# Kernel tuning notes

Measured on AMD Instinct MI355X. Metric: run time of the kernel, lower is better.

The kernel has to match this reference:

```python
import jax, jax.numpy as jnp
import numpy as np

N = 50000
E = 800000
IN_CH = 128
HID = 64
HEADS = 4
NEG_SLOPE_GAT = 0.2   # PyG GATConv default negative_slope
NEG_SLOPE_ACT = 0.01  # nn.LeakyReLU default
LN_EPS = 1e-5


def segment_softmax(logits, seg, num):
    # softmax over edges grouped by destination node (PyG softmax semantics)
    m = jax.ops.segment_max(logits, seg, num_segments=num)
    m = jnp.where(jnp.isfinite(m), m, 0.0)
    e = jnp.exp(logits - m[seg])
    s = jax.ops.segment_sum(e, seg, num_segments=num)
    return e / (s[seg] + 1e-16)


def gat_conv(x, edge_index, W, a_src, a_dst, b, heads, out_ch):
    n = x.shape[0]
    loop = jnp.arange(n)
    src = jnp.concatenate([edge_index[0], loop])  # message sources (x_j)
    dst = jnp.concatenate([edge_index[1], loop])  # aggregation targets (x_i)
    h = (x @ W).reshape(n, heads, out_ch)          # [N,H,C]
    alpha_src = (h * a_src).sum(-1)                # [N,H]
    alpha_dst = (h * a_dst).sum(-1)                # [N,H]
    alpha = alpha_src[src] + alpha_dst[dst]        # [E',H]
    alpha = jax.nn.leaky_relu(alpha, NEG_SLOPE_GAT)
    alpha = segment_softmax(alpha, dst, n)
    msg = h[src] * alpha[:, :, None]               # [E',H,C] gathered messages
    out = jax.ops.segment_sum(msg, dst, num_segments=n)  # [N,H,C]
    return out.reshape(n, heads * out_ch) + b


def layer_norm(x, gamma, beta):
    mu = x.mean(-1, keepdims=True)
    var = ((x - mu) ** 2).mean(-1, keepdims=True)
    return (x - mu) * jax.lax.rsqrt(var + LN_EPS) * gamma + beta


def setup_inputs() -> dict:
    key = jax.random.key(0)
    ks = jax.random.split(key, 12)
    d1 = HEADS * HID
    inp = {
        "x": jax.random.normal(ks[0], (N, IN_CH), dtype=jnp.float32),
        "edge_index": jax.random.randint(ks[1], (2, E), 0, N, dtype=jnp.int64),
        "W1": jax.random.normal(ks[2], (IN_CH, d1), dtype=jnp.float32) * 0.05,
        "a_src1": jax.random.normal(ks[3], (HEADS, HID), dtype=jnp.float32) * 0.1,
        "a_dst1": jax.random.normal(ks[4], (HEADS, HID), dtype=jnp.float32) * 0.1,
        "b1": jnp.zeros((d1,), dtype=jnp.float32),
        "gamma": jnp.ones((d1,), dtype=jnp.float32),
        "beta": jnp.zeros((d1,), dtype=jnp.float32),
        "W2": jax.random.normal(ks[5], (d1, HID), dtype=jnp.float32) * 0.05,
        "a_src2": jax.random.normal(ks[6], (1, HID), dtype=jnp.float32) * 0.1,
        "a_dst2": jax.random.normal(ks[7], (1, HID), dtype=jnp.float32) * 0.1,
        "b2": jnp.zeros((HID,), dtype=jnp.float32),
    }
    return inp


def reference(x, edge_index, W1, a_src1, a_dst1, b1, gamma, beta, W2, a_src2, a_dst2, b2):
    h = gat_conv(x, edge_index, W1, a_src1, a_dst1, b1, HEADS, HID)  # [N, H*HID]
    h = layer_norm(h, gamma, beta)
    h = jax.nn.leaky_relu(h, NEG_SLOPE_ACT)
    out = gat_conv(h, edge_index, W2, a_src2, a_dst2, b2, 1, HID)    # [N, HID]
    return out
```

## Files before the change

### kernel.cpp

```cpp
#include <hip/hip_runtime.h>
#include <hip/hip_bf16.h>

#define IN_CH 128
#define D1 256
#define HID 64
#define HEADS 4
#define SCAN_BLK 1024

typedef _Float16 h16;
typedef __attribute__((ext_vector_type(4))) _Float16 half4v;
typedef __attribute__((ext_vector_type(8))) _Float16 half8v;
typedef __attribute__((ext_vector_type(4))) float f32x4;

__device__ __forceinline__ float lrelu02(float v) { return v > 0.f ? v : 0.2f * v; }
__device__ __forceinline__ float lrelu001(float v) { return v > 0.f ? v : 0.01f * v; }

__global__ __launch_bounds__(256) void setup_kernel(const float* __restrict__ W1,
                                                    const float* __restrict__ W2,
                                                    const float* __restrict__ a_src1,
                                                    const float* __restrict__ a_dst1,
                                                    const float* __restrict__ a_src2,
                                                    const float* __restrict__ a_dst2,
                                                    const int* __restrict__ ei,
                                                    int* __restrict__ cnt,
                                                    h16* __restrict__ w1t,
                                                    h16* __restrict__ w2t,
                                                    int nE) {
    const int b = blockIdx.x;
    const int t = threadIdx.x;
    if (b == 0) {
        for (int k = 0; k < IN_CH; ++k) w1t[t * IN_CH + k] = (h16)W1[k * D1 + t];
    } else if (b == 1) {
        if (t < HID)
            for (int k = 0; k < D1; ++k) w2t[t * D1 + k] = (h16)W2[k * HID + t];
        for (int i = t; i < 14 * D1; i += 256) w2t[66 * D1 + i] = (h16)0.f;
    } else if (b == 2) {
        for (int o = t; o < 1024; o += 256) {
            int v = o >> 7, k = o & 127;
            int h = v & 3;
            const float* avec = (v >> 2) ? (a_dst1 + h * HID) : (a_src1 + h * HID);
            const float* wrow = W1 + k * D1 + h * HID;
            float s = 0.f;
            for (int c = 0; c < HID; ++c) s += wrow[c] * avec[c];
            w1t[(256 + v) * IN_CH + k] = (h16)s;
            w1t[(264 + v) * IN_CH + k] = (h16)0.f;
        }
    } else if (b == 3) {
        for (int o = t; o < 512; o += 256) {
            int v = o >> 8, k = o & 255;
            const float* avec = v ? a_dst2 : a_src2;
            const float* wrow = W2 + k * HID;
            float s = 0.f;
            for (int c = 0; c < HID; ++c) s += wrow[c] * avec[c];
            w2t[(64 + v) * D1 + k] = (h16)s;
        }
    } else {
        int e = (b - 4) * 256 + t;
        if (e < nE) atomicAdd(&cnt[ei[nE + e]], 1);
    }
}

__global__ __launch_bounds__(256) void scan1_kernel(const int* __restrict__ cnt,
                                                    int* __restrict__ pre,
                                                    int* __restrict__ blockSums, int n) {
    __shared__ int lds[256];
    const int t = threadIdx.x;
    const int base = blockIdx.x * SCAN_BLK + t * 4;
    int v0 = 0, v1 = 0, v2 = 0, v3 = 0;
    if (base + 0 < n) v0 = cnt[base + 0];
    if (base + 1 < n) v1 = cnt[base + 1];
    if (base + 2 < n) v2 = cnt[base + 2];
    if (base + 3 < n) v3 = cnt[base + 3];
    int s = v0 + v1 + v2 + v3;
    lds[t] = s;
    __syncthreads();
    for (int off = 1; off < 256; off <<= 1) {
        int x = 0;
        if (t >= off) x = lds[t - off];
        __syncthreads();
        if (t >= off) lds[t] += x;
        __syncthreads();
    }
    int excl = lds[t] - s;
    if (t == 255) blockSums[blockIdx.x] = lds[255];
    if (base + 0 < n) pre[base + 0] = excl;
    if (base + 1 < n) pre[base + 1] = excl + v0;
    if (base + 2 < n) pre[base + 2] = excl + v0 + v1;
    if (base + 3 < n) pre[base + 3] = excl + v0 + v1 + v2;
}

__global__ __launch_bounds__(256) void scan23_kernel(int* __restrict__ pre,
                                                     const int* __restrict__ blockSums,
                                                     int* __restrict__ cursor,
                                                     int n, int nE, int nb) {
    __shared__ int soff_s;
    const int t = threadIdx.x;
    if (t < 64) {
        int v = (t < blockIdx.x && t < nb) ? blockSums[t] : 0;
        #pragma unroll
        for (int off = 1; off < 64; off <<= 1) v += __shfl_xor(v, off, 64);
        if (t == 0) soff_s = v;
    }
    __syncthreads();
    const int soff = soff_s;
    const int base = blockIdx.x * SCAN_BLK + t * 4;
    #pragma unroll
    for (int q = 0; q < 4; ++q) {
        int i = base + q;
        if (i < n) {
            int v = pre[i] + soff;
            pre[i] = v;
            cursor[i] = v;
        }
    }
    if (blockIdx.x == 0 && t == 0) pre[n] = nE;
}

__global__ __launch_bounds__(256) void scatter_ewt_kernel(const int* __restrict__ ei,
                                                          int* __restrict__ cursor,
                                                          const float* __restrict__ asad,
                                                          int* __restrict__ srcIdx,
                                                          h16* __restrict__ wE1, int nE) {
    int e = blockIdx.x * 256 + threadIdx.x;
    if (e >= nE) return;
    int src = ei[e];
    int dst = ei[nE + e];
    int pos = atomicAdd(&cursor[dst], 1);
    srcIdx[pos] = src;
    float4 as = *(const float4*)&asad[(size_t)src * 8];
    float4 ad = *(const float4*)&asad[(size_t)dst * 8 + 4];
    half4v w;
    w.x = (h16)expf(lrelu02(as.x + ad.x));
    w.y = (h16)expf(lrelu02(as.y + ad.y));
    w.z = (h16)expf(lrelu02(as.z + ad.z));
    w.w = (h16)expf(lrelu02(as.w + ad.w));
    *(half4v*)&wE1[(size_t)pos * 4] = w;
}

__global__ __launch_bounds__(256) void gemm1_mfma(const float* __restrict__ x,
                                                  const h16* __restrict__ w1t,
                                                  h16* __restrict__ h1,
                                                  float* __restrict__ asad, int n) {
    const int wave = threadIdx.x >> 6, lane = threadIdx.x & 63;
    const int r = lane & 15, ksel = lane >> 4;
    const int rowBase = blockIdx.x * 64 + wave * 16;
    const int row_a = rowBase + r;
    half8v a[4];
    if (row_a < n) {
        const float* xrow = x + (size_t)row_a * IN_CH + ksel * 8;
        #pragma unroll
        for (int kk = 0; kk < 4; ++kk) {
            float4 u = *(const float4*)(xrow + kk * 32);
            float4 v = *(const float4*)(xrow + kk * 32 + 4);
            half8v av;
            av[0] = (h16)u.x; av[1] = (h16)u.y; av[2] = (h16)u.z; av[3] = (h16)u.w;
            av[4] = (h16)v.x; av[5] = (h16)v.y; av[6] = (h16)v.z; av[7] = (h16)v.w;
            a[kk] = av;
        }
    } else {
        #pragma unroll
        for (int kk = 0; kk < 4; ++kk) a[kk] = (half8v){};
    }
    f32x4 acc[17];
    #pragma unroll
    for (int ct = 0; ct < 17; ++ct) acc[ct] = (f32x4){0.f, 0.f, 0.f, 0.f};
    #pragma unroll
    for (int ct = 0; ct < 17; ++ct) {
        const h16* wrow = w1t + (size_t)(ct * 16 + r) * IN_CH + ksel * 8;
        #pragma unroll
        for (int kk = 0; kk < 4; ++kk) {
            half8v b = *(const half8v*)(wrow + kk * 32);
            acc[ct] = __builtin_amdgcn_mfma_f32_16x16x32_f16(a[kk], b, acc[ct], 0, 0, 0);
        }
    }
    #pragma unroll
    for (int i = 0; i < 4; ++i) {
        int row = rowBase + ksel * 4 + i;
        if (row < n) {
            #pragma unroll
            for (int ct = 0; ct < 16; ++ct)
                h1[(size_t)row * D1 + ct * 16 + r] = (h16)acc[ct][i];
            if (r < 8) asad[(size_t)row * 8 + r] = acc[16][i];
        }
    }
}

__global__ __launch_bounds__(256) void gemm2_mfma(const h16* __restrict__ hm,
                                                  const h16* __restrict__ w2t,
                                                  h16* __restrict__ h2,
                                                  float* __restrict__ asad2, int n) {
    const int wave = threadIdx.x >> 6, lane = threadIdx.x & 63;
    const int r = lane & 15, ksel = lane >> 4;
    const int rowBase = blockIdx.x * 64 + wave * 16;
    const h16* xrow = hm + (size_t)(rowBase + r) * D1 + ksel * 8;
    half8v a[8];
    #pragma unroll
    for (int kk = 0; kk < 8; ++kk) a[kk] = *(const half8v*)(xrow + kk * 32);
    f32x4 acc[5];
    #pragma unroll
    for (int ct = 0; ct < 5; ++ct) acc[ct] = (f32x4){0.f, 0.f, 0.f, 0.f};
    #pragma unroll
    for (int ct = 0; ct < 5; ++ct) {
        const h16* wrow = w2t + (size_t)(ct * 16 + r) * D1 + ksel * 8;
        #pragma unroll
        for (int kk = 0; kk < 8; ++kk) {
            half8v b = *(const half8v*)(wrow + kk * 32);
            acc[ct] = __builtin_amdgcn_mfma_f32_16x16x32_f16(a[kk], b, acc[ct], 0, 0, 0);
        }
    }
    #pragma unroll
    for (int i = 0; i < 4; ++i) {
        int row = rowBase + ksel * 4 + i;
        if (row < n) {
            #pragma unroll
            for (int ct = 0; ct < 4; ++ct)
                h2[(size_t)row * HID + ct * 16 + r] = (h16)acc[ct][i];
            if (r < 2) asad2[(size_t)row * 2 + r] = acc[4][i];
        }
    }
}

__global__ __launch_bounds__(256) void gather1_kernel(const h16* __restrict__ h1,
                                                      const float* __restrict__ asad,
                                                      const h16* __restrict__ wE1,
                                                      const int* __restrict__ rowStart,
                                                      const int* __restrict__ srcIdx,
                                                      const float* __restrict__ b1,
                                                      const float* __restrict__ gamma,
                                                      const float* __restrict__ beta,
                                                      h16* __restrict__ hmid, int n, int npad) {
    const int lane = threadIdx.x & 63;
    const int node = (blockIdx.x * 256 + threadIdx.x) >> 6;
    if (node >= npad) return;
    if (node >= n) {
        half4v z = {};
        *(half4v*)&hmid[(size_t)node * D1 + lane * 4] = z;
        return;
    }
    const int hh = lane >> 4;
    const float w = expf(lrelu02(asad[(size_t)node * 8 + hh] +
                                 asad[(size_t)node * 8 + 4 + hh]));
    half4v sv = *(const half4v*)&h1[(size_t)node * D1 + lane * 4];
    float4 acc = make_float4((float)sv.x * w, (float)sv.y * w,
                             (float)sv.z * w, (float)sv.w * w);
    float den = w;
    const int beg = rowStart[node], end = rowStart[node + 1];
    int j = beg;
    for (; j + 7 < end; j += 8) {
        int sI[8]; float wv[8]; half4v rv[8];
        #pragma unroll
        for (int q = 0; q < 8; ++q) sI[q] = srcIdx[j + q];
        #pragma unroll
        for (int q = 0; q < 8; ++q) wv[q] = (float)wE1[(size_t)(j + q) * 4 + hh];
        #pragma unroll
        for (int q = 0; q < 8; ++q) rv[q] = *(const half4v*)&h1[(size_t)sI[q] * D1 + lane * 4];
        #pragma unroll
        for (int q = 0; q < 8; ++q) {
            acc.x = fmaf((float)rv[q].x, wv[q], acc.x);
            acc.y = fmaf((float)rv[q].y, wv[q], acc.y);
            acc.z = fmaf((float)rv[q].z, wv[q], acc.z);
            acc.w = fmaf((float)rv[q].w, wv[q], acc.w);
            den += wv[q];
        }
    }
    for (; j + 3 < end; j += 4) {
        int sI[4]; float wv[4]; half4v rv[4];
        #pragma unroll
        for (int q = 0; q < 4; ++q) sI[q] = srcIdx[j + q];
        #pragma unroll
        for (int q = 0; q < 4; ++q) wv[q] = (float)wE1[(size_t)(j + q) * 4 + hh];
        #pragma unroll
        for (int q = 0; q < 4; ++q) rv[q] = *(const half4v*)&h1[(size_t)sI[q] * D1 + lane * 4];
        #pragma unroll
        for (int q = 0; q < 4; ++q) {
            acc.x = fmaf((float)rv[q].x, wv[q], acc.x);
            acc.y = fmaf((float)rv[q].y, wv[q], acc.y);
            acc.z = fmaf((float)rv[q].z, wv[q], acc.z);
            acc.w = fmaf((float)rv[q].w, wv[q], acc.w);
            den += wv[q];
        }
    }
    for (; j < end; ++j) {
        int s = srcIdx[j];
        float wj = (float)wE1[(size_t)j * 4 + hh];
        half4v xv = *(const half4v*)&h1[(size_t)s * D1 + lane * 4];
        acc.x = fmaf((float)xv.x, wj, acc.x);
        acc.y = fmaf((float)xv.y, wj, acc.y);
        acc.z = fmaf((float)xv.z, wj, acc.z);
        acc.w = fmaf((float)xv.w, wj, acc.w);
        den += wj;
    }
    float inv = 1.f / (den + 1e-16f);
    float4 bv = *(const float4*)&b1[lane * 4];
    float4 y;
    y.x = acc.x * inv + bv.x; y.y = acc.y * inv + bv.y;
    y.z = acc.z * inv + bv.z; y.w = acc.w * inv + bv.w;
    float s = y.x + y.y + y.z + y.w;
    #pragma unroll
    for (int off = 1; off < 64; off <<= 1) s += __shfl_xor(s, off, 64);
    float mu = s * (1.f / 256.f);
    float4 dx;
    dx.x = y.x - mu; dx.y = y.y - mu; dx.z = y.z - mu; dx.w = y.w - mu;
    float sq = dx.x * dx.x + dx.y * dx.y + dx.z * dx.z + dx.w * dx.w;
    #pragma unroll
    for (int off = 1; off < 64; off <<= 1) sq += __shfl_xor(sq, off, 64);
    float rs = rsqrtf(sq * (1.f / 256.f) + 1e-5f);
    float4 g = *(const float4*)&gamma[lane * 4];
    float4 be = *(const float4*)&beta[lane * 4];
    half4v o;
    o.x = (h16)lrelu001(dx.x * rs * g.x + be.x);
    o.y = (h16)lrelu001(dx.y * rs * g.y + be.y);
    o.z = (h16)lrelu001(dx.z * rs * g.z + be.z);
    o.w = (h16)lrelu001(dx.w * rs * g.w + be.w);
    *(half4v*)&hmid[(size_t)node * D1 + lane * 4] = o;
}

__global__ __launch_bounds__(256) void gather2_kernel(const h16* __restrict__ h2,
                                                      const float* __restrict__ asad2,
                                                      const int* __restrict__ rowStart,
                                                      const int* __restrict__ srcIdx,
                                                      const float* __restrict__ b2,
                                                      float* __restrict__ out, int n) {
    const int lane = threadIdx.x & 63;
    const int node = (blockIdx.x * 256 + threadIdx.x) >> 6;
    if (node >= n) return;
    const int li = lane & 15, eh = lane >> 4;
    const int c0 = li * 4;
    const float ad_n = asad2[(size_t)node * 2 + 1];
    float acc[4] = {0.f, 0.f, 0.f, 0.f};
    float den = 0.f;
    if (eh == 0) {
        float w0 = expf(lrelu02(asad2[(size_t)node * 2] + ad_n));
        half4v sv = *(const half4v*)&h2[(size_t)node * HID + c0];
        #pragma unroll
        for (int i = 0; i < 4; ++i) acc[i] = (float)sv[i] * w0;
        den = w0;
    }
    const int beg = rowStart[node], end = rowStart[node + 1];
    int j = beg;
    for (; j + 7 < end; j += 8) {
        int e0 = j + eh, e1 = j + 4 + eh;
        int s0 = srcIdx[e0], s1 = srcIdx[e1];
        float a0 = asad2[(size_t)s0 * 2], a1 = asad2[(size_t)s1 * 2];
        half4v r0 = *(const half4v*)&h2[(size_t)s0 * HID + c0];
        half4v r1 = *(const half4v*)&h2[(size_t)s1 * HID + c0];
        float w0 = expf(lrelu02(a0 + ad_n));
        float w1 = expf(lrelu02(a1 + ad_n));
        #pragma unroll
        for (int i = 0; i < 4; ++i) {
            acc[i] = fmaf((float)r0[i], w0, acc[i]);
            acc[i] = fmaf((float)r1[i], w1, acc[i]);
        }
        den += w0 + w1;
    }
    for (; j < end; j += 4) {
        int e = j + eh;
        bool v = e < end;
        int s = v ? srcIdx[e] : 0;
        float w = v ? expf(lrelu02(asad2[(size_t)s * 2] + ad_n)) : 0.f;
        half4v r = *(const half4v*)&h2[(size_t)s * HID + c0];
        #pragma unroll
        for (int i = 0; i < 4; ++i) acc[i] = fmaf((float)r[i], w, acc[i]);
        den += w;
    }
    #pragma unroll
    for (int i = 0; i < 4; ++i) {
        acc[i] += __shfl_xor(acc[i], 32, 64);
        acc[i] += __shfl_xor(acc[i], 16, 64);
    }
    den += __shfl_xor(den, 32, 64);
    den += __shfl_xor(den, 16, 64);
    if (lane < 16) {
        float inv = 1.f / (den + 1e-16f);
        float4 bv = *(const float4*)&b2[c0];
        float4 o;
        o.x = acc[0] * inv + bv.x;
        o.y = acc[1] * inv + bv.y;
        o.z = acc[2] * inv + bv.z;
        o.w = acc[3] * inv + bv.w;
        *(float4*)&out[(size_t)node * HID + c0] = o;
    }
}

extern "C" void kernel_launch(void* const* d_in, const int* in_sizes, int n_in,
                              void* d_out, int out_size, void* d_ws, size_t ws_size,
                              hipStream_t stream) {
    const float* x      = (const float*)d_in[0];
    const int*   ei     = (const int*)d_in[1];
    const float* W1     = (const float*)d_in[2];
    const float* a_src1 = (const float*)d_in[3];
    const float* a_dst1 = (const float*)d_in[4];
    const float* b1     = (const float*)d_in[5];
    const float* gamma  = (const float*)d_in[6];
    const float* beta   = (const float*)d_in[7];
    const float* W2     = (const float*)d_in[8];
    const float* a_src2 = (const float*)d_in[9];
    const float* a_dst2 = (const float*)d_in[10];
    const float* b2     = (const float*)d_in[11];
    float* out = (float*)d_out;

    const int N = in_sizes[0] / IN_CH;
    const int E = in_sizes[1] / 2;
    const int NP = (N + 63) & ~63;

    float* ws = (float*)d_ws;
    size_t off = 0;
    h16*   h1   = (h16*)(ws + off); off += (size_t)128 * N;
    h16*   hmid = (h16*)(ws + off); off += (size_t)128 * NP;
    h16*   h2   = (h16*)(ws + off); off += (size_t)32 * N;
    float* asad = ws + off;         off += (size_t)8 * N;
    float* asad2= ws + off;         off += (size_t)2 * N;
    h16*   wE1  = (h16*)(ws + off); off += (size_t)2 * E;
    int* srcIdx    = (int*)(ws + off); off += E;
    int* rowStart  = (int*)(ws + off); off += N + 1;
    int* cursor    = (int*)(ws + off); off += N;
    int* blockSums = (int*)(ws + off); off += 64;
    h16* w1t = (h16*)(ws + off); off += 17408;
    h16* w2t = (h16*)(ws + off); off += 10240;

    const int nodeBlocks  = (N + 3) / 4;
    const int nodeBlocksP = (NP + 3) / 4;
    const int nThreadBlocksE = (E + 255) / 256;
    const int scanBlocks = (N + SCAN_BLK - 1) / SCAN_BLK;

    hipMemsetAsync(cursor, 0, (size_t)N * 4, stream);
    setup_kernel<<<4 + nThreadBlocksE, 256, 0, stream>>>(
        W1, W2, a_src1, a_dst1, a_src2, a_dst2, ei, cursor, w1t, w2t, E);
    scan1_kernel<<<scanBlocks, 256, 0, stream>>>(cursor, rowStart, blockSums, N);
    scan23_kernel<<<scanBlocks, 256, 0, stream>>>(rowStart, blockSums, cursor, N, E, scanBlocks);

    gemm1_mfma<<<NP / 64, 256, 0, stream>>>(x, w1t, h1, asad, N);
    scatter_ewt_kernel<<<nThreadBlocksE, 256, 0, stream>>>(ei, cursor, asad, srcIdx, wE1, E);
    gather1_kernel<<<nodeBlocksP, 256, 0, stream>>>(h1, asad, wE1, rowStart, srcIdx,
                                                    b1, gamma, beta, hmid, N, NP);
    gemm2_mfma<<<NP / 64, 256, 0, stream>>>(hmid, w2t, h2, asad2, N);
    gather2_kernel<<<nodeBlocks, 256, 0, stream>>>(h2, asad2, rowStart, srcIdx,
                                                   b2, out, N);
}
```

Measured before the change: 261.6 us.

## Pad CSR rows to multiples of four, fuse scan with gemm1, use fp16 gather accumulation

Each destination row in the CSR is padded to a multiple of four edges. Padding slots point to a dummy node n, whose zeroed features and -1e30 logit make its weight vanish, so the gather loops can use vector int4 index loads with no tail predication. The scan fixup kernel and the gemm1 kernel are merged into one launch. Edge weights move to a head-major layout so half4 weight loads are contiguous. Gather1 accumulates products and the denominator in packed fp16 to cut ALU work, which risks precision loss and overflow for high-degree nodes. The memset grows to clear the padded index and weight buffers.

```diff
diff --git a/kernel.cpp b/kernel.cpp
--- a/kernel.cpp
+++ b/kernel.cpp
@@ -67,10 +67,10 @@
     const int t = threadIdx.x;
     const int base = blockIdx.x * SCAN_BLK + t * 4;
     int v0 = 0, v1 = 0, v2 = 0, v3 = 0;
-    if (base + 0 < n) v0 = cnt[base + 0];
-    if (base + 1 < n) v1 = cnt[base + 1];
-    if (base + 2 < n) v2 = cnt[base + 2];
-    if (base + 3 < n) v3 = cnt[base + 3];
+    if (base + 0 < n) v0 = (cnt[base + 0] + 3) & ~3;
+    if (base + 1 < n) v1 = (cnt[base + 1] + 3) & ~3;
+    if (base + 2 < n) v2 = (cnt[base + 2] + 3) & ~3;
+    if (base + 3 < n) v3 = (cnt[base + 3] + 3) & ~3;
     int s = v0 + v1 + v2 + v3;
     lds[t] = s;
     __syncthreads();
@@ -89,38 +89,94 @@
     if (base + 3 < n) pre[base + 3] = excl + v0 + v1 + v2;
 }
 
-__global__ __launch_bounds__(256) void scan23_kernel(int* __restrict__ pre,
-                                                     const int* __restrict__ blockSums,
-                                                     int* __restrict__ cursor,
-                                                     int n, int nE, int nb) {
-    __shared__ int soff_s;
-    const int t = threadIdx.x;
-    if (t < 64) {
-        int v = (t < blockIdx.x && t < nb) ? blockSums[t] : 0;
-        #pragma unroll
-        for (int off = 1; off < 64; off <<= 1) v += __shfl_xor(v, off, 64);
-        if (t == 0) soff_s = v;
-    }
-    __syncthreads();
-    const int soff = soff_s;
-    const int base = blockIdx.x * SCAN_BLK + t * 4;
-    #pragma unroll
-    for (int q = 0; q < 4; ++q) {
-        int i = base + q;
-        if (i < n) {
-            int v = pre[i] + soff;
-            pre[i] = v;
-            cursor[i] = v;
-        }
-    }
-    if (blockIdx.x == 0 && t == 0) pre[n] = nE;
+__global__ __launch_bounds__(256) void scan23_gemm1_kernel(
+        int* __restrict__ pre, const int* __restrict__ blockSums,
+        int* __restrict__ cursor, int* __restrict__ srcIdx,
+        float* __restrict__ asad2, int n, int nbScan,
+        const float* __restrict__ x, const h16* __restrict__ w1t,
+        h16* __restrict__ h1, float* __restrict__ asad) {
+    if (blockIdx.x < (unsigned)nbScan) {
+        __shared__ int soff_s;
+        const int t = threadIdx.x;
+        if (t < 64) {
+            int v = (t < (int)blockIdx.x && t < nbScan) ? blockSums[t] : 0;
+            #pragma unroll
+            for (int off = 1; off < 64; off <<= 1) v += __shfl_xor(v, off, 64);
+            if (t == 0) soff_s = v;
+        }
+        __syncthreads();
+        const int soff = soff_s;
+        const int base = blockIdx.x * SCAN_BLK + t * 4;
+        #pragma unroll
+        for (int q = 0; q < 4; ++q) {
+            int i = base + q;
+            if (i < n) {
+                int d = cursor[i];
+                int v = pre[i] + soff;
+                pre[i] = v;
+                cursor[i] = v;
+                int dp = (d + 3) & ~3;
+                for (int p = d; p < dp; ++p) srcIdx[v + p] = n;
+                if (i == n - 1) pre[n] = v + dp;
+            }
+        }
+        if (blockIdx.x == 0 && t == 0) {
+            asad2[(size_t)n * 2] = -1e30f;
+            asad2[(size_t)n * 2 + 1] = -1e30f;
+        }
+        return;
+    }
+    const int bid = blockIdx.x - nbScan;
+    const int wave = threadIdx.x >> 6, lane = threadIdx.x & 63;
+    const int r = lane & 15, ksel = lane >> 4;
+    const int rowBase = bid * 64 + wave * 16;
+    const int row_a = rowBase + r;
+    half8v a[4];
+    if (row_a < n) {
+        const float* xrow = x + (size_t)row_a * IN_CH + ksel * 8;
+        #pragma unroll
+        for (int kk = 0; kk < 4; ++kk) {
+            float4 u = *(const float4*)(xrow + kk * 32);
+            float4 v = *(const float4*)(xrow + kk * 32 + 4);
+            half8v av;
+            av[0] = (h16)u.x; av[1] = (h16)u.y; av[2] = (h16)u.z; av[3] = (h16)u.w;
+            av[4] = (h16)v.x; av[5] = (h16)v.y; av[6] = (h16)v.z; av[7] = (h16)v.w;
+            a[kk] = av;
+        }
+    } else {
+        #pragma unroll
+        for (int kk = 0; kk < 4; ++kk) a[kk] = (half8v){};
+    }
+    f32x4 acc[17];
+    #pragma unroll
+    for (int ct = 0; ct < 17; ++ct) acc[ct] = (f32x4){0.f, 0.f, 0.f, 0.f};
+    #pragma unroll
+    for (int ct = 0; ct < 17; ++ct) {
+        const h16* wrow = w1t + (size_t)(ct * 16 + r) * IN_CH + ksel * 8;
+        #pragma unroll
+        for (int kk = 0; kk < 4; ++kk) {
+            half8v b = *(const half8v*)(wrow + kk * 32);
+            acc[ct] = __builtin_amdgcn_mfma_f32_16x16x32_f16(a[kk], b, acc[ct], 0, 0, 0);
+        }
+    }
+    #pragma unroll
+    for (int i = 0; i < 4; ++i) {
+        int row = rowBase + ksel * 4 + i;
+        if (row < n) {
+            #pragma unroll
+            for (int ct = 0; ct < 16; ++ct)
+                h1[(size_t)row * D1 + ct * 16 + r] = (h16)acc[ct][i];
+            if (r < 8) asad[(size_t)row * 8 + r] = acc[16][i];
+        }
+    }
 }
 
 __global__ __launch_bounds__(256) void scatter_ewt_kernel(const int* __restrict__ ei,
                                                           int* __restrict__ cursor,
                                                           const float* __restrict__ asad,
                                                           int* __restrict__ srcIdx,
-                                                          h16* __restrict__ wE1, int nE) {
+                                                          h16* __restrict__ wE1,
+                                                          int nE, int Epad) {
     int e = blockIdx.x * 256 + threadIdx.x;
     if (e >= nE) return;
     int src = ei[e];
@@ -129,60 +185,10 @@
     srcIdx[pos] = src;
     float4 as = *(const float4*)&asad[(size_t)src * 8];
     float4 ad = *(const float4*)&asad[(size_t)dst * 8 + 4];
-    half4v w;
-    w.x = (h16)expf(lrelu02(as.x + ad.x));
-    w.y = (h16)expf(lrelu02(as.y + ad.y));
-    w.z = (h16)expf(lrelu02(as.z + ad.z));
-    w.w = (h16)expf(lrelu02(as.w + ad.w));
-    *(half4v*)&wE1[(size_t)pos * 4] = w;
-}
-
-__global__ __launch_bounds__(256) void gemm1_mfma(const float* __restrict__ x,
-                                                  const h16* __restrict__ w1t,
-                                                  h16* __restrict__ h1,
-                                                  float* __restrict__ asad, int n) {
-    const int wave = threadIdx.x >> 6, lane = threadIdx.x & 63;
-    const int r = lane & 15, ksel = lane >> 4;
-    const int rowBase = blockIdx.x * 64 + wave * 16;
-    const int row_a = rowBase + r;
-    half8v a[4];
-    if (row_a < n) {
-        const float* xrow = x + (size_t)row_a * IN_CH + ksel * 8;
-        #pragma unroll
-        for (int kk = 0; kk < 4; ++kk) {
-            float4 u = *(const float4*)(xrow + kk * 32);
-            float4 v = *(const float4*)(xrow + kk * 32 + 4);
-            half8v av;
-            av[0] = (h16)u.x; av[1] = (h16)u.y; av[2] = (h16)u.z; av[3] = (h16)u.w;
-            av[4] = (h16)v.x; av[5] = (h16)v.y; av[6] = (h16)v.z; av[7] = (h16)v.w;
-            a[kk] = av;
-        }
-    } else {
-        #pragma unroll
-        for (int kk = 0; kk < 4; ++kk) a[kk] = (half8v){};
-    }
-    f32x4 acc[17];
-    #pragma unroll
-    for (int ct = 0; ct < 17; ++ct) acc[ct] = (f32x4){0.f, 0.f, 0.f, 0.f};
-    #pragma unroll
-    for (int ct = 0; ct < 17; ++ct) {
-        const h16* wrow = w1t + (size_t)(ct * 16 + r) * IN_CH + ksel * 8;
-        #pragma unroll
-        for (int kk = 0; kk < 4; ++kk) {
-            half8v b = *(const half8v*)(wrow + kk * 32);
-            acc[ct] = __builtin_amdgcn_mfma_f32_16x16x32_f16(a[kk], b, acc[ct], 0, 0, 0);
-        }
-    }
-    #pragma unroll
-    for (int i = 0; i < 4; ++i) {
-        int row = rowBase + ksel * 4 + i;
-        if (row < n) {
-            #pragma unroll
-            for (int ct = 0; ct < 16; ++ct)
-                h1[(size_t)row * D1 + ct * 16 + r] = (h16)acc[ct][i];
-            if (r < 8) asad[(size_t)row * 8 + r] = acc[16][i];
-        }
-    }
+    wE1[(size_t)0 * Epad + pos] = (h16)expf(lrelu02(as.x + ad.x));
+    wE1[(size_t)1 * Epad + pos] = (h16)expf(lrelu02(as.y + ad.y));
+    wE1[(size_t)2 * Epad + pos] = (h16)expf(lrelu02(as.z + ad.z));
+    wE1[(size_t)3 * Epad + pos] = (h16)expf(lrelu02(as.w + ad.w));
 }
 
 __global__ __launch_bounds__(256) void gemm2_mfma(const h16* __restrict__ hm,
@@ -228,7 +234,8 @@
                                                       const float* __restrict__ b1,
                                                       const float* __restrict__ gamma,
                                                       const float* __restrict__ beta,
-                                                      h16* __restrict__ hmid, int n, int npad) {
+                                                      h16* __restrict__ hmid,
+                                                      int n, int npad, int Epad) {
     const int lane = threadIdx.x & 63;
     const int node = (blockIdx.x * 256 + threadIdx.x) >> 6;
     if (node >= npad) return;
@@ -238,63 +245,60 @@
         return;
     }
     const int hh = lane >> 4;
-    const float w = expf(lrelu02(asad[(size_t)node * 8 + hh] +
-                                 asad[(size_t)node * 8 + 4 + hh]));
+    const float wself = expf(lrelu02(asad[(size_t)node * 8 + hh] +
+                                     asad[(size_t)node * 8 + 4 + hh]));
     half4v sv = *(const half4v*)&h1[(size_t)node * D1 + lane * 4];
-    float4 acc = make_float4((float)sv.x * w, (float)sv.y * w,
-                             (float)sv.z * w, (float)sv.w * w);
-    float den = w;
+    h16 wsh = (h16)wself;
+    half4v acc = sv * (half4v){wsh, wsh, wsh, wsh};
+    float den = wself;
+    half4v den4 = {};
+    const h16* wp = wE1 + (size_t)hh * Epad;
     const int beg = rowStart[node], end = rowStart[node + 1];
     int j = beg;
-    for (; j + 7 < end; j += 8) {
-        int sI[8]; float wv[8]; half4v rv[8];
-        #pragma unroll
-        for (int q = 0; q < 8; ++q) sI[q] = srcIdx[j + q];
-        #pragma unroll
-        for (int q = 0; q < 8; ++q) wv[q] = (float)wE1[(size_t)(j + q) * 4 + hh];
-        #pragma unroll
-        for (int q = 0; q < 8; ++q) rv[q] = *(const half4v*)&h1[(size_t)sI[q] * D1 + lane * 4];
-        #pragma unroll
-        for (int q = 0; q < 8; ++q) {
-            acc.x = fmaf((float)rv[q].x, wv[q], acc.x);
-            acc.y = fmaf((float)rv[q].y, wv[q], acc.y);
-            acc.z = fmaf((float)rv[q].z, wv[q], acc.z);
-            acc.w = fmaf((float)rv[q].w, wv[q], acc.w);
-            den += wv[q];
-        }
-    }
-    for (; j + 3 < end; j += 4) {
-        int sI[4]; float wv[4]; half4v rv[4];
-        #pragma unroll
-        for (int q = 0; q < 4; ++q) sI[q] = srcIdx[j + q];
-        #pragma unroll
-        for (int q = 0; q < 4; ++q) wv[q] = (float)wE1[(size_t)(j + q) * 4 + hh];
-        #pragma unroll
-        for (int q = 0; q < 4; ++q) rv[q] = *(const half4v*)&h1[(size_t)sI[q] * D1 + lane * 4];
-        #pragma unroll
-        for (int q = 0; q < 4; ++q) {
-            acc.x = fmaf((float)rv[q].x, wv[q], acc.x);
-            acc.y = fmaf((float)rv[q].y, wv[q], acc.y);
-            acc.z = fmaf((float)rv[q].z, wv[q], acc.z);
-            acc.w = fmaf((float)rv[q].w, wv[q], acc.w);
-            den += wv[q];
-        }
-    }
-    for (; j < end; ++j) {
-        int s = srcIdx[j];
-        float wj = (float)wE1[(size_t)j * 4 + hh];
-        half4v xv = *(const half4v*)&h1[(size_t)s * D1 + lane * 4];
-        acc.x = fmaf((float)xv.x, wj, acc.x);
-        acc.y = fmaf((float)xv.y, wj, acc.y);
-        acc.z = fmaf((float)xv.z, wj, acc.z);
-        acc.w = fmaf((float)xv.w, wj, acc.w);
-        den += wj;
-    }
+    for (; j + 8 <= end; j += 8) {
+        int4 ia = *(const int4*)&srcIdx[j];
+        int4 ib = *(const int4*)&srcIdx[j + 4];
+        half4v wa = *(const half4v*)&wp[j];
+        half4v wb = *(const half4v*)&wp[j + 4];
+        half4v r0 = *(const half4v*)&h1[(size_t)ia.x * D1 + lane * 4];
+        half4v r1 = *(const half4v*)&h1[(size_t)ia.y * D1 + lane * 4];
+        half4v r2 = *(const half4v*)&h1[(size_t)ia.z * D1 + lane * 4];
+        half4v r3 = *(const half4v*)&h1[(size_t)ia.w * D1 + lane * 4];
+        half4v r4 = *(const half4v*)&h1[(size_t)ib.x * D1 + lane * 4];
+        half4v r5 = *(const half4v*)&h1[(size_t)ib.y * D1 + lane * 4];
+        half4v r6 = *(const half4v*)&h1[(size_t)ib.z * D1 + lane * 4];
+        half4v r7 = *(const half4v*)&h1[(size_t)ib.w * D1 + lane * 4];
+        acc += r0 * (half4v){wa[0], wa[0], wa[0], wa[0]};
+        acc += r1 * (half4v){wa[1], wa[1], wa[1], wa[1]};
+        acc += r2 * (half4v){wa[2], wa[2], wa[2], wa[2]};
+        acc += r3 * (half4v){wa[3], wa[3], wa[3], wa[3]};
+        acc += r4 * (half4v){wb[0], wb[0], wb[0], wb[0]};
+        acc += r5 * (half4v){wb[1], wb[1], wb[1], wb[1]};
+        acc += r6 * (half4v){wb[2], wb[2], wb[2], wb[2]};
+        acc += r7 * (half4v){wb[3], wb[3], wb[3], wb[3]};
+        den4 += wa;
+        den4 += wb;
+    }
+    if (j < end) {
+        int4 ia = *(const int4*)&srcIdx[j];
+        half4v wa = *(const half4v*)&wp[j];
+        half4v r0 = *(const half4v*)&h1[(size_t)ia.x * D1 + lane * 4];
+        half4v r1 = *(const half4v*)&h1[(size_t)ia.y * D1 + lane * 4];
+        half4v r2 = *(const half4v*)&h1[(size_t)ia.z * D1 + lane * 4];
+        half4v r3 = *(const half4v*)&h1[(size_t)ia.w * D1 + lane * 4];
+        acc += r0 * (half4v){wa[0], wa[0], wa[0], wa[0]};
+        acc += r1 * (half4v){wa[1], wa[1], wa[1], wa[1]};
+        acc += r2 * (half4v){wa[2], wa[2], wa[2], wa[2]};
+        acc += r3 * (half4v){wa[3], wa[3], wa[3], wa[3]};
+        den4 += wa;
+    }
+    den += (float)den4[0] + (float)den4[1] + (float)den4[2] + (float)den4[3];
+    float4 accf = make_float4((float)acc[0], (float)acc[1], (float)acc[2], (float)acc[3]);
     float inv = 1.f / (den + 1e-16f);
     float4 bv = *(const float4*)&b1[lane * 4];
     float4 y;
-    y.x = acc.x * inv + bv.x; y.y = acc.y * inv + bv.y;
-    y.z = acc.z * inv + bv.z; y.w = acc.w * inv + bv.w;
+    y.x = accf.x * inv + bv.x; y.y = accf.y * inv + bv.y;
+    y.z = accf.z * inv + bv.z; y.w = accf.w * inv + bv.w;
     float s = y.x + y.y + y.z + y.w;
     #pragma unroll
     for (int off = 1; off < 64; off <<= 1) s += __shfl_xor(s, off, 64);
@@ -338,7 +342,7 @@
     }
     const int beg = rowStart[node], end = rowStart[node + 1];
     int j = beg;
-    for (; j + 7 < end; j += 8) {
+    for (; j + 8 <= end; j += 8) {
         int e0 = j + eh, e1 = j + 4 + eh;
         int s0 = srcIdx[e0], s1 = srcIdx[e1];
         float a0 = asad2[(size_t)s0 * 2], a1 = asad2[(size_t)s1 * 2];
@@ -353,11 +357,10 @@
         }
         den += w0 + w1;
     }
-    for (; j < end; j += 4) {
+    if (j < end) {
         int e = j + eh;
-        bool v = e < end;
-        int s = v ? srcIdx[e] : 0;
-        float w = v ? expf(lrelu02(asad2[(size_t)s * 2] + ad_n)) : 0.f;
+        int s = srcIdx[e];
+        float w = expf(lrelu02(asad2[(size_t)s * 2] + ad_n));
         half4v r = *(const half4v*)&h2[(size_t)s * HID + c0];
         #pragma unroll
         for (int i = 0; i < 4; ++i) acc[i] = fmaf((float)r[i], w, acc[i]);
@@ -402,37 +405,41 @@
     const int N = in_sizes[0] / IN_CH;
     const int E = in_sizes[1] / 2;
     const int NP = (N + 63) & ~63;
+    const int Emax = E + 3 * N + 16;
+    const int Epad = (Emax + 15) & ~15;
 
     float* ws = (float*)d_ws;
     size_t off = 0;
-    h16*   h1   = (h16*)(ws + off); off += (size_t)128 * N;
+    h16*   h1   = (h16*)(ws + off); off += (size_t)128 * (N + 1);
     h16*   hmid = (h16*)(ws + off); off += (size_t)128 * NP;
-    h16*   h2   = (h16*)(ws + off); off += (size_t)32 * N;
+    h16*   h2   = (h16*)(ws + off); off += (size_t)32 * (N + 1);
     float* asad = ws + off;         off += (size_t)8 * N;
-    float* asad2= ws + off;         off += (size_t)2 * N;
-    h16*   wE1  = (h16*)(ws + off); off += (size_t)2 * E;
-    int* srcIdx    = (int*)(ws + off); off += E;
+    float* asad2= ws + off;         off += (size_t)2 * (N + 1);
     int* rowStart  = (int*)(ws + off); off += N + 1;
-    int* cursor    = (int*)(ws + off); off += N;
     int* blockSums = (int*)(ws + off); off += 64;
     h16* w1t = (h16*)(ws + off); off += 17408;
     h16* w2t = (h16*)(ws + off); off += 10240;
+    int* cursor = (int*)(ws + off); off += N;
+    int* srcIdx = (int*)(ws + off); off += Emax;
+    h16* wE1    = (h16*)(ws + off); off += (size_t)2 * Epad;
+    const size_t memsetBytes = ((size_t)N + Emax) * 4 + (size_t)4 * Epad * 2;
 
     const int nodeBlocks  = (N + 3) / 4;
     const int nodeBlocksP = (NP + 3) / 4;
     const int nThreadBlocksE = (E + 255) / 256;
     const int scanBlocks = (N + SCAN_BLK - 1) / SCAN_BLK;
 
-    hipMemsetAsync(cursor, 0, (size_t)N * 4, stream);
+    hipMemsetAsync(cursor, 0, memsetBytes, stream);
     setup_kernel<<<4 + nThreadBlocksE, 256, 0, stream>>>(
         W1, W2, a_src1, a_dst1, a_src2, a_dst2, ei, cursor, w1t, w2t, E);
     scan1_kernel<<<scanBlocks, 256, 0, stream>>>(cursor, rowStart, blockSums, N);
-    scan23_kernel<<<scanBlocks, 256, 0, stream>>>(rowStart, blockSums, cursor, N, E, scanBlocks);
-
-    gemm1_mfma<<<NP / 64, 256, 0, stream>>>(x, w1t, h1, asad, N);
-    scatter_ewt_kernel<<<nThreadBlocksE, 256, 0, stream>>>(ei, cursor, asad, srcIdx, wE1, E);
+    scan23_gemm1_kernel<<<scanBlocks + NP / 64, 256, 0, stream>>>(
+        rowStart, blockSums, cursor, srcIdx, asad2, N, scanBlocks,
+        x, w1t, h1, asad);
+    scatter_ewt_kernel<<<nThreadBlocksE, 256, 0, stream>>>(ei, cursor, asad, srcIdx,
+                                                           wE1, E, Epad);
     gather1_kernel<<<nodeBlocksP, 256, 0, stream>>>(h1, asad, wE1, rowStart, srcIdx,
-                                                    b1, gamma, beta, hmid, N, NP);
+                                                    b1, gamma, beta, hmid, N, NP, Epad);
     gemm2_mfma<<<NP / 64, 256, 0, stream>>>(hmid, w2t, h2, asad2, N);
     gather2_kernel<<<nodeBlocks, 256, 0, stream>>>(h2, asad2, rowStart, srcIdx,
                                                    b2, out, N);
```

After: 277.6 us. 1.06x slower.
